# Optimization experiments

Hardware: AMD Instinct MI355X
Metric: run time of the kernel (lower is better)

## Reference

```python
import jax, jax.numpy as jnp
import numpy as np

B, S, D, H = 2, 4096, 512, 8
DK = D // H

def setup_inputs() -> dict:
    key = jax.random.key(0)
    ks = jax.random.split(key, 11)
    s = 1.0 / np.sqrt(D)
    return {
        "q": jax.random.normal(ks[0], (B, S, D), jnp.float32),
        "k": jax.random.normal(ks[1], (B, S, D), jnp.float32),
        "v": jax.random.normal(ks[2], (B, S, D), jnp.float32),
        "Wq": jax.random.normal(ks[3], (D, D), jnp.float32) * s,
        "bq": jax.random.normal(ks[4], (D,), jnp.float32) * s,
        "Wk": jax.random.normal(ks[5], (D, D), jnp.float32) * s,
        "bk": jax.random.normal(ks[6], (D,), jnp.float32) * s,
        "Wv": jax.random.normal(ks[7], (D, D), jnp.float32) * s,
        "bv": jax.random.normal(ks[8], (D,), jnp.float32) * s,
        "Wo": jax.random.normal(ks[9], (D, D), jnp.float32) * s,
        "bo": jax.random.normal(ks[10], (D,), jnp.float32) * s,
    }

def reference(q, k, v, Wq, bq, Wk, bk, Wv, bv, Wo, bo):
    bs = q.shape[0]
    # torch Linear: x @ W.T + b ; then split heads [B,S,H,DK] -> [B,H,S,DK]
    qh = (q @ Wq.T + bq).reshape(bs, -1, H, DK).transpose(0, 2, 1, 3)
    kh = (k @ Wk.T + bk).reshape(bs, -1, H, DK).transpose(0, 2, 1, 3)
    vh = (v @ Wv.T + bv).reshape(bs, -1, H, DK).transpose(0, 2, 1, 3)
    scores = jnp.einsum("bhqd,bhkd->bhqk", qh, kh) / jnp.sqrt(jnp.float32(DK))
    attn = jax.nn.softmax(scores, axis=-1)  # [B,H,S,S] materialized, like torch
    out = jnp.einsum("bhqk,bhkd->bhqd", attn, vh)
    concat = out.transpose(0, 2, 1, 3).reshape(bs, -1, D)
    return concat @ Wo.T + bo
```

## Files before the change

### kernel.cpp

```cpp
#include <hip/hip_runtime.h>
#include <hip/hip_bf16.h>

#define NHEAD 8
#define DKH 64
#define DMODEL 512
#define SEQ 4096
#define BATCH 2
#define MROWS (BATCH * SEQ)

using bf16x8 = __attribute__((ext_vector_type(8))) short;
using s16x4  = __attribute__((ext_vector_type(4))) short;
using f32x4  = __attribute__((ext_vector_type(4))) float;
using f32x16 = __attribute__((ext_vector_type(16))) float;

__device__ __forceinline__ float b2f(unsigned short u) {
    union { unsigned short u; __hip_bfloat16 h; } c; c.u = u; return __bfloat162float(c.h);
}
__device__ __forceinline__ short rhu(float x) {
    union { float f; unsigned u; } c; c.f = x;
    return (short)((c.u + 0x8000u) >> 16);
}

__device__ __forceinline__ unsigned cvtpk(float lo, float hi) {
    unsigned r;
    asm("v_cvt_pk_bf16_f32 %0, %1, %2" : "=v"(r) : "v"(lo), "v"(hi));
    return r;
}

#if __has_builtin(__builtin_amdgcn_exp2f)
#define EXP2F(x) __builtin_amdgcn_exp2f(x)
#else
#define EXP2F(x) exp2f(x)
#endif

template <bool F32>
__device__ __forceinline__ bf16x8 ld8(const void* p, size_t eidx) {
    if (F32) {
        const float* f = (const float*)p + eidx;
        float4 a = *(const float4*)f;
        float4 b = *(const float4*)(f + 4);
        union { unsigned u[4]; bf16x8 v; } t;
        t.u[0] = cvtpk(a.x, a.y);
        t.u[1] = cvtpk(a.z, a.w);
        t.u[2] = cvtpk(b.x, b.y);
        t.u[3] = cvtpk(b.z, b.w);
        return t.v;
    }
    return *(const bf16x8*)((const short*)p + eidx);
}

template <int EPI, int TM, bool F32A, bool F32W>
__device__ __forceinline__ void gemm_core(const void* __restrict__ A,
                                          const void* __restrict__ W,
                                          const void* __restrict__ bias,
                                          void* __restrict__ out,
                                          int bm, int bn) {
    constexpr int MT = TM / 32;
    __shared__ __align__(16) short lA[TM * 72];
    __shared__ __align__(16) short lB[128 * 72];

    const int tid  = threadIdx.x;
    const int lane = tid & 63;
    const int w    = tid >> 6;
    const int wr = w >> 1, wc = w & 1;
    const int g = lane >> 4, ln = lane & 15;

    const f32x4 zero = {0.f, 0.f, 0.f, 0.f};
    f32x4 acc[MT][4];
    for (int mt = 0; mt < MT; mt++)
        for (int nt = 0; nt < 4; nt++) acc[mt][nt] = zero;

    for (int kb = 0; kb < DMODEL; kb += 64) {
        for (int i = 0; i < TM / 32; i++) {
            int vv = tid + i * 256;
            int row = vv >> 3, cv = vv & 7;
            *(bf16x8*)&lA[row * 72 + cv * 8] =
                ld8<F32A>(A, (size_t)(bm + row) * DMODEL + kb + cv * 8);
        }
        for (int i = 0; i < 4; i++) {
            int vv = tid + i * 256;
            int row = vv >> 3, cv = vv & 7;
            *(bf16x8*)&lB[row * 72 + cv * 8] =
                ld8<F32W>(W, (size_t)(bn + row) * DMODEL + kb + cv * 8);
        }
        __syncthreads();

        for (int ks = 0; ks < 2; ks++) {
            const int ko = ks * 32 + g * 8;
            bf16x8 af[MT], bf[4];
            for (int mt = 0; mt < MT; mt++)
                af[mt] = *(const bf16x8*)&lA[(wr * 16 * MT + mt * 16 + ln) * 72 + ko];
            for (int nt = 0; nt < 4; nt++)
                bf[nt] = *(const bf16x8*)&lB[(wc * 64 + nt * 16 + ln) * 72 + ko];
            for (int mt = 0; mt < MT; mt++)
                for (int nt = 0; nt < 4; nt++)
                    acc[mt][nt] = __builtin_amdgcn_mfma_f32_16x16x32_bf16(
                        af[mt], bf[nt], acc[mt][nt], 0, 0, 0);
        }
        __syncthreads();
    }

    if (EPI == 2) {
        for (int mt = 0; mt < MT; mt++) {
            for (int r = 0; r < 4; r++) {
                const int m = bm + wr * 16 * MT + mt * 16 + g * 4 + r;
                const float bz = ((const float*)bias)[m];
                const int hh = m >> 6, dk = m & 63;
                for (int nt = 0; nt < 4; nt++) {
                    const int n = bn + wc * 64 + nt * 16 + ln;
                    const int bb = n >> 12, s = n & 4095;
                    const int sl = s & 127, sh = s & ~127;
                    const int kt = sl >> 5, kk = sl & 31;
                    const int t = kk >> 3, hb = (kk >> 2) & 1, lo = kk & 3;
                    const int kappa = kt * 32 + (t >> 1) * 16 + hb * 8 + (t & 1) * 4 + lo;
                    ((short*)out)[(((size_t)(bb * NHEAD + hh)) * DKH + dk) * SEQ + sh + kappa] =
                        rhu(acc[mt][nt][r] + bz);
                }
            }
        }
    } else {
        for (int nt = 0; nt < 4; nt++) {
            const int n = bn + wc * 64 + nt * 16 + ln;
            const float bz = ((const float*)bias)[n];
            for (int mt = 0; mt < MT; mt++) {
                for (int r = 0; r < 4; r++) {
                    const int m = bm + wr * 16 * MT + mt * 16 + g * 4 + r;
                    const float val = acc[mt][nt][r] + bz;
                    if (EPI == 1) {
                        const int bb = m >> 12, s = m & 4095;
                        const int hh = n >> 6, dk = n & 63;
                        ((short*)out)[(((size_t)(bb * NHEAD + hh)) * SEQ + s) * DKH + dk] =
                            rhu(val);
                    } else {
                        ((float*)out)[(size_t)m * DMODEL + n] = val;
                    }
                }
            }
        }
    }
}

__global__ __launch_bounds__(256) void qkv_kernel(
    const float* __restrict__ q, const float* __restrict__ k, const float* __restrict__ v,
    const float* __restrict__ Wq, const float* __restrict__ bq,
    const float* __restrict__ Wk, const float* __restrict__ bk,
    const float* __restrict__ Wv, const float* __restrict__ bv,
    short* __restrict__ Qh, short* __restrict__ Kh, short* __restrict__ Vt) {
    if (blockIdx.z == 0) {
        gemm_core<1, 128, true, true>(q, Wq, bq, Qh, blockIdx.x * 128, blockIdx.y * 128);
    } else if (blockIdx.z == 1) {
        gemm_core<1, 128, true, true>(k, Wk, bk, Kh, blockIdx.x * 128, blockIdx.y * 128);
    } else {
        gemm_core<2, 128, true, true>(Wv, v, bv, Vt, blockIdx.y * 128, blockIdx.x * 128);
    }
}

__global__ __launch_bounds__(256) void oproj_kernel(
    const short* __restrict__ A, const float* __restrict__ W,
    const float* __restrict__ bias, float* __restrict__ out) {
    gemm_core<0, 64, false, true>(A, W, bias, out, blockIdx.x * 64, blockIdx.y * 128);
}

__global__ __launch_bounds__(256, 4) void attn_kernel(
    const short* __restrict__ Qh, const short* __restrict__ Kh,
    const short* __restrict__ Vt, short* __restrict__ concat) {
    const int tid  = threadIdx.x;
    const int lane = tid & 63;
    const int w    = tid >> 6;
    const int c  = lane & 31;
    const int h5 = lane >> 5;
    const int qsel = w & 1;
    const int ksel = w >> 1;
    const int bh = blockIdx.y;
    const int b = bh >> 3, h = bh & 7;
    const int qq = blockIdx.x * 64 + qsel * 32 + c;

    const short* Qp = Qh + (size_t)bh * SEQ * DKH;
    const short* Kp = Kh + (size_t)bh * SEQ * DKH;
    const short* Vp = Vt + (size_t)bh * DKH * SEQ;

    __shared__ __align__(16) char smem[35840];
    short* lK = (short*)smem;
    short* lV = (short*)(smem + 18432);
    float* cO = (float*)smem;
    float* cL = (float*)(smem + 32768);

    const float QS = 0.125f * 1.44269504f;
    bf16x8 qf[4];
    for (int ks = 0; ks < 4; ks++) {
        bf16x8 raw = *(const bf16x8*)&Qp[(size_t)qq * DKH + ks * 16 + h5 * 8];
        union { unsigned u[4]; bf16x8 v; } t;
        for (int j = 0; j < 4; j++)
            t.u[j] = cvtpk(b2f((unsigned short)raw[2 * j]) * QS,
                           b2f((unsigned short)raw[2 * j + 1]) * QS);
        qf[ks] = t.v;
    }

    float l_self = 0.f;
    f32x16 o_acc[2];
    for (int dt = 0; dt < 2; dt++)
        for (int r = 0; r < 16; r++) o_acc[dt][r] = 0.f;

    for (int kb = 0; kb < SEQ; kb += 128) {
        for (int i = 0; i < 4; i++) {
            int vv = tid + i * 256;
            {
                int row = vv >> 3, cv = vv & 7;
                *(bf16x8*)&lK[row * 72 + cv * 8] =
                    *(const bf16x8*)&Kp[(size_t)(kb + row) * DKH + cv * 8];
            }
            {
                int dk = vv >> 4, kc = vv & 15;
                *(bf16x8*)&lV[dk * 136 + kc * 8] =
                    *(const bf16x8*)&Vp[(size_t)dk * SEQ + kb + kc * 8];
            }
        }
        __syncthreads();

        f32x16 st[2];
        for (int kt = 0; kt < 2; kt++)
            for (int r = 0; r < 16; r++) st[kt][r] = -12.f;
        for (int ks = 0; ks < 4; ks++)
            for (int kt = 0; kt < 2; kt++) {
                bf16x8 kf = *(const bf16x8*)&lK[(ksel * 64 + kt * 32 + c) * 72 + ks * 16 + h5 * 8];
                st[kt] = __builtin_amdgcn_mfma_f32_32x32x16_bf16(kf, qf[ks], st[kt], 0, 0, 0);
            }

        for (int kt = 0; kt < 2; kt++)
            for (int r = 0; r < 16; r++) {
                float p = EXP2F(st[kt][r]);
                st[kt][r] = p;
                l_self += p;
            }

        for (int ks2 = 0; ks2 < 4; ks2++) {
            const int kt = ks2 >> 1, ob = 8 * (ks2 & 1);
            union { unsigned u[4]; bf16x8 v; } pf;
            for (int j = 0; j < 4; j++)
                pf.u[j] = cvtpk(st[kt][ob + 2 * j], st[kt][ob + 2 * j + 1]);
            const int colg = (ksel * 4 + ks2) * 16 + h5 * 8;
            for (int dt = 0; dt < 2; dt++) {
                bf16x8 vf = *(const bf16x8*)&lV[(dt * 32 + c) * 136 + colg];
                o_acc[dt] = __builtin_amdgcn_mfma_f32_32x32x16_bf16(vf, pf.v, o_acc[dt], 0, 0, 0);
            }
        }
        __syncthreads();
    }

    const float half_l = l_self + __shfl_xor(l_self, 32);
    if (ksel == 1) {
        for (int dt = 0; dt < 2; dt++)
            for (int r = 0; r < 16; r++)
                cO[(((qsel * 2 + dt) * 16 + r) * 2 + h5) * 32 + c] = o_acc[dt][r];
        if (h5 == 0) cL[qsel * 32 + c] = half_l;
    }
    __syncthreads();
    if (ksel == 0) {
        const float l = half_l + cL[qsel * 32 + c];
        const float inv = 1.0f / l;
        short* crow = concat + ((size_t)(b * SEQ + qq)) * DMODEL + h * DKH;
        for (int dt = 0; dt < 2; dt++)
            for (int j2 = 0; j2 < 4; j2++) {
                const int r = j2 * 4;
                float o0 = (o_acc[dt][r + 0] + cO[(((qsel * 2 + dt) * 16 + r + 0) * 2 + h5) * 32 + c]) * inv;
                float o1 = (o_acc[dt][r + 1] + cO[(((qsel * 2 + dt) * 16 + r + 1) * 2 + h5) * 32 + c]) * inv;
                float o2 = (o_acc[dt][r + 2] + cO[(((qsel * 2 + dt) * 16 + r + 2) * 2 + h5) * 32 + c]) * inv;
                float o3 = (o_acc[dt][r + 3] + cO[(((qsel * 2 + dt) * 16 + r + 3) * 2 + h5) * 32 + c]) * inv;
                union { unsigned u[2]; s16x4 v; } pk;
                pk.u[0] = cvtpk(o0, o1);
                pk.u[1] = cvtpk(o2, o3);
                const int dk = dt * 32 + 8 * j2 + 4 * h5;
                *(s16x4*)&crow[dk] = pk.v;
            }
    }
}

extern "C" void kernel_launch(void* const* d_in, const int* in_sizes, int n_in,
                              void* d_out, int out_size, void* d_ws, size_t ws_size,
                              hipStream_t stream) {
    const float* q  = (const float*)d_in[0];
    const float* k  = (const float*)d_in[1];
    const float* v  = (const float*)d_in[2];
    const float* Wq = (const float*)d_in[3];
    const float* bq = (const float*)d_in[4];
    const float* Wk = (const float*)d_in[5];
    const float* bk = (const float*)d_in[6];
    const float* Wv = (const float*)d_in[7];
    const float* bv = (const float*)d_in[8];
    const float* Wo = (const float*)d_in[9];
    const float* bo = (const float*)d_in[10];

    const size_t nElemH = (size_t)BATCH * NHEAD * SEQ * DKH;
    short* Qh     = (short*)d_ws;
    short* Kh     = Qh + nElemH;
    short* Vt     = Kh + nElemH;
    short* concat = Vt + nElemH;

    dim3 blk(256);
    qkv_kernel<<<dim3(MROWS / 128, DMODEL / 128, 3), blk, 0, stream>>>(
        q, k, v, Wq, bq, Wk, bk, Wv, bv, Qh, Kh, Vt);
    attn_kernel<<<dim3(SEQ / 64, BATCH * NHEAD), blk, 0, stream>>>(Qh, Kh, Vt, concat);
    oproj_kernel<<<dim3(MROWS / 64, DMODEL / 128), blk, 0, stream>>>(
        concat, Wo, bo, (float*)d_out);
}
```

Measured before the change: 240.6 us.

## Pre-convert inputs to bf16 and load GEMM tiles via direct global-to-LDS

Adds a separate conversion pass that turns the fp32 activations and all weight matrices into bf16 buffers in the workspace. The projection GEMMs then read bf16 and stage tiles with global_load_lds 16-byte direct-to-LDS loads, using an XOR-swizzled unpadded LDS layout instead of padded rows. The goal is to cut register staging and the repeated fp32-to-bf16 conversion that each GEMM block did for every tile, since the weights were converted many times over. The cost is an extra kernel launch plus a full fp32 read and bf16 write of the inputs. The concat buffer now reuses the q bf16 region.

```diff
diff --git a/kernel.cpp b/kernel.cpp
--- a/kernel.cpp
+++ b/kernel.cpp
@@ -33,37 +33,62 @@
 #define EXP2F(x) exp2f(x)
 #endif
 
-template <bool F32>
-__device__ __forceinline__ bf16x8 ld8(const void* p, size_t eidx) {
-    if (F32) {
-        const float* f = (const float*)p + eidx;
-        float4 a = *(const float4*)f;
-        float4 b = *(const float4*)(f + 4);
-        union { unsigned u[4]; bf16x8 v; } t;
-        t.u[0] = cvtpk(a.x, a.y);
-        t.u[1] = cvtpk(a.z, a.w);
-        t.u[2] = cvtpk(b.x, b.y);
-        t.u[3] = cvtpk(b.z, b.w);
-        return t.v;
-    }
-    return *(const bf16x8*)((const short*)p + eidx);
-}
-
-template <int EPI, int TM, bool F32A, bool F32W>
-__device__ __forceinline__ void gemm_core(const void* __restrict__ A,
-                                          const void* __restrict__ W,
-                                          const void* __restrict__ bias,
+__device__ __forceinline__ void gload_lds16(const void* g, void* l) {
+    __builtin_amdgcn_global_load_lds(
+        (const __attribute__((address_space(1))) void*)g,
+        (__attribute__((address_space(3))) void*)l,
+        16, 0, 0);
+}
+
+#define QG ((size_t)MROWS * DMODEL / 8)
+#define WG ((size_t)DMODEL * DMODEL / 8)
+
+__global__ __launch_bounds__(256) void convert_kernel(
+    const float* __restrict__ q, const float* __restrict__ k, const float* __restrict__ v,
+    const float* __restrict__ Wq, const float* __restrict__ Wk,
+    const float* __restrict__ Wv, const float* __restrict__ Wo,
+    short* __restrict__ dst) {
+    const size_t i = (size_t)blockIdx.x * 256 + threadIdx.x;
+    const float* src;
+    size_t off;
+    if (i < 3 * QG) {
+        size_t s = i / QG;
+        off = (i - s * QG) * 8;
+        src = (s == 0) ? q : (s == 1) ? k : v;
+    } else {
+        size_t j = i - 3 * QG;
+        size_t s = j / WG;
+        off = (j - s * WG) * 8;
+        src = (s == 0) ? Wq : (s == 1) ? Wk : (s == 2) ? Wv : Wo;
+    }
+    float4 a = *(const float4*)(src + off);
+    float4 b = *(const float4*)(src + off + 4);
+    union { unsigned u[4]; bf16x8 v8; } t;
+    t.u[0] = cvtpk(a.x, a.y);
+    t.u[1] = cvtpk(a.z, a.w);
+    t.u[2] = cvtpk(b.x, b.y);
+    t.u[3] = cvtpk(b.z, b.w);
+    *(bf16x8*)&dst[i * 8] = t.v8;
+}
+
+template <int EPI, int TM>
+__device__ __forceinline__ void gemm_core(const short* __restrict__ A,
+                                          const short* __restrict__ W,
+                                          const float* __restrict__ bias,
                                           void* __restrict__ out,
                                           int bm, int bn) {
     constexpr int MT = TM / 32;
-    __shared__ __align__(16) short lA[TM * 72];
-    __shared__ __align__(16) short lB[128 * 72];
+    constexpr int AI = TM / 32;
+    __shared__ __align__(128) short lA[TM * 64];
+    __shared__ __align__(128) short lB[128 * 64];
 
     const int tid  = threadIdx.x;
     const int lane = tid & 63;
     const int w    = tid >> 6;
     const int wr = w >> 1, wc = w & 1;
     const int g = lane >> 4, ln = lane & 15;
+    const int l8 = lane >> 3, cb = lane & 7;
+    const int sw8 = cb ^ l8;
 
     const f32x4 zero = {0.f, 0.f, 0.f, 0.f};
     f32x4 acc[MT][4];
@@ -71,27 +96,29 @@
         for (int nt = 0; nt < 4; nt++) acc[mt][nt] = zero;
 
     for (int kb = 0; kb < DMODEL; kb += 64) {
-        for (int i = 0; i < TM / 32; i++) {
-            int vv = tid + i * 256;
-            int row = vv >> 3, cv = vv & 7;
-            *(bf16x8*)&lA[row * 72 + cv * 8] =
-                ld8<F32A>(A, (size_t)(bm + row) * DMODEL + kb + cv * 8);
+        for (int i = 0; i < AI; i++) {
+            const int rb = w * (8 * AI) + i * 8;
+            gload_lds16(&A[(size_t)(bm + rb + l8) * DMODEL + kb + sw8 * 8],
+                        &lA[rb * 64]);
         }
         for (int i = 0; i < 4; i++) {
-            int vv = tid + i * 256;
-            int row = vv >> 3, cv = vv & 7;
-            *(bf16x8*)&lB[row * 72 + cv * 8] =
-                ld8<F32W>(W, (size_t)(bn + row) * DMODEL + kb + cv * 8);
+            const int rb = w * 32 + i * 8;
+            gload_lds16(&W[(size_t)(bn + rb + l8) * DMODEL + kb + sw8 * 8],
+                        &lB[rb * 64]);
         }
         __syncthreads();
 
         for (int ks = 0; ks < 2; ks++) {
-            const int ko = ks * 32 + g * 8;
+            const int xr = (ks * 4 + g) ^ (ln & 7);
             bf16x8 af[MT], bf[4];
-            for (int mt = 0; mt < MT; mt++)
-                af[mt] = *(const bf16x8*)&lA[(wr * 16 * MT + mt * 16 + ln) * 72 + ko];
-            for (int nt = 0; nt < 4; nt++)
-                bf[nt] = *(const bf16x8*)&lB[(wc * 64 + nt * 16 + ln) * 72 + ko];
+            for (int mt = 0; mt < MT; mt++) {
+                const int row = wr * 16 * MT + mt * 16 + ln;
+                af[mt] = *(const bf16x8*)&lA[row * 64 + xr * 8];
+            }
+            for (int nt = 0; nt < 4; nt++) {
+                const int row = wc * 64 + nt * 16 + ln;
+                bf[nt] = *(const bf16x8*)&lB[row * 64 + xr * 8];
+            }
             for (int mt = 0; mt < MT; mt++)
                 for (int nt = 0; nt < 4; nt++)
                     acc[mt][nt] = __builtin_amdgcn_mfma_f32_16x16x32_bf16(
@@ -141,24 +168,23 @@
 }
 
 __global__ __launch_bounds__(256) void qkv_kernel(
-    const float* __restrict__ q, const float* __restrict__ k, const float* __restrict__ v,
-    const float* __restrict__ Wq, const float* __restrict__ bq,
-    const float* __restrict__ Wk, const float* __restrict__ bk,
-    const float* __restrict__ Wv, const float* __restrict__ bv,
+    const short* __restrict__ qb, const short* __restrict__ kb, const short* __restrict__ vb,
+    const short* __restrict__ Wqb, const short* __restrict__ Wkb, const short* __restrict__ Wvb,
+    const float* __restrict__ bq, const float* __restrict__ bk, const float* __restrict__ bv,
     short* __restrict__ Qh, short* __restrict__ Kh, short* __restrict__ Vt) {
     if (blockIdx.z == 0) {
-        gemm_core<1, 128, true, true>(q, Wq, bq, Qh, blockIdx.x * 128, blockIdx.y * 128);
+        gemm_core<1, 128>(qb, Wqb, bq, Qh, blockIdx.x * 128, blockIdx.y * 128);
     } else if (blockIdx.z == 1) {
-        gemm_core<1, 128, true, true>(k, Wk, bk, Kh, blockIdx.x * 128, blockIdx.y * 128);
+        gemm_core<1, 128>(kb, Wkb, bk, Kh, blockIdx.x * 128, blockIdx.y * 128);
     } else {
-        gemm_core<2, 128, true, true>(Wv, v, bv, Vt, blockIdx.y * 128, blockIdx.x * 128);
+        gemm_core<2, 128>(Wvb, vb, bv, Vt, blockIdx.y * 128, blockIdx.x * 128);
     }
 }
 
 __global__ __launch_bounds__(256) void oproj_kernel(
-    const short* __restrict__ A, const float* __restrict__ W,
+    const short* __restrict__ A, const short* __restrict__ W,
     const float* __restrict__ bias, float* __restrict__ out) {
-    gemm_core<0, 64, false, true>(A, W, bias, out, blockIdx.x * 64, blockIdx.y * 128);
+    gemm_core<0, 64>(A, W, bias, out, blockIdx.x * 64, blockIdx.y * 128);
 }
 
 __global__ __launch_bounds__(256, 4) void attn_kernel(
@@ -291,15 +317,25 @@
     const float* bo = (const float*)d_in[10];
 
     const size_t nElemH = (size_t)BATCH * NHEAD * SEQ * DKH;
-    short* Qh     = (short*)d_ws;
-    short* Kh     = Qh + nElemH;
-    short* Vt     = Kh + nElemH;
-    short* concat = Vt + nElemH;
+    const size_t nElemW = (size_t)DMODEL * DMODEL;
+    short* Qh    = (short*)d_ws;
+    short* Kh    = Qh + nElemH;
+    short* Vt    = Kh + nElemH;
+    short* bfbuf = Vt + nElemH;
+    short* qb    = bfbuf;
+    short* kb    = qb + nElemH;
+    short* vb    = kb + nElemH;
+    short* Wqb   = vb + nElemH;
+    short* Wkb   = Wqb + nElemW;
+    short* Wvb   = Wkb + nElemW;
+    short* Wob   = Wvb + nElemW;
+    short* concat = qb;
 
     dim3 blk(256);
+    convert_kernel<<<dim3(6656), blk, 0, stream>>>(q, k, v, Wq, Wk, Wv, Wo, bfbuf);
     qkv_kernel<<<dim3(MROWS / 128, DMODEL / 128, 3), blk, 0, stream>>>(
-        q, k, v, Wq, bq, Wk, bk, Wv, bv, Qh, Kh, Vt);
+        qb, kb, vb, Wqb, Wkb, Wvb, bq, bk, bv, Qh, Kh, Vt);
     attn_kernel<<<dim3(SEQ / 64, BATCH * NHEAD), blk, 0, stream>>>(Qh, Kh, Vt, concat);
     oproj_kernel<<<dim3(MROWS / 64, DMODEL / 128), blk, 0, stream>>>(
-        concat, Wo, bo, (float*)d_out);
-}
+        concat, Wob, bo, (float*)d_out);
+}
```

Measured after the change: 230.4 us. 4.3% less time.
